# Performance work log

Hardware: AMD Instinct MI355X
Metric: run time of the kernel (lower is better)

Reference implementation:

```python
import jax, jax.numpy as jnp
import numpy as np

HSIZE = 128
E = 640000


def _init_linear(key, fan_in, fan_out):
    # torch nn.Linear default init: U(-1/sqrt(fan_in), 1/sqrt(fan_in))
    kw, kb = jax.random.split(key)
    bound = 1.0 / np.sqrt(fan_in)
    W = jax.random.uniform(kw, (fan_in, fan_out), jnp.float32, -bound, bound)
    b = jax.random.uniform(kb, (fan_out,), jnp.float32, -bound, bound)
    return W, b


def setup_inputs() -> dict:
    key = jax.random.key(0)
    ks = jax.random.split(key, 6)
    hself = jax.random.normal(ks[0], (E, HSIZE), jnp.float32)
    hother = jax.random.normal(ks[1], (E, HSIZE), jnp.float32)
    Wm1, bm1 = _init_linear(ks[2], 2 * HSIZE, HSIZE)
    Wm2, bm2 = _init_linear(ks[3], HSIZE, HSIZE)
    Wu1, bu1 = _init_linear(ks[4], 2 * HSIZE, HSIZE)
    Wu2, bu2 = _init_linear(ks[5], HSIZE, HSIZE)
    return {"hself": hself, "hother": hother,
            "Wm1": Wm1, "bm1": bm1, "Wm2": Wm2, "bm2": bm2,
            "Wu1": Wu1, "bu1": bu1, "Wu2": Wu2, "bu2": bu2}


def _mlp2(a, b, W1, b1, W2, b2):
    # concat([a, b], -1) @ W1 done without materializing the concat
    h = a @ W1[:HSIZE] + b @ W1[HSIZE:] + b1
    h = jax.nn.relu(h)
    return h @ W2 + b2


def reference(hself, hother, Wm1, bm1, Wm2, bm2, Wu1, bu1, Wu2, bu2):
    # msg: Linear(2h,h) -> ReLU -> Linear(h,h) on cat([hself, hother])
    msg = _mlp2(hself, hother, Wm1, bm1, Wm2, bm2)
    # upd: Linear(2h,h) -> ReLU -> Linear(h,h) on cat([hself, msg])
    out = _mlp2(hself, msg, Wu1, bu1, Wu2, bu2)
    return out
```

## Files before the change

### kernel.cpp

```cpp
#include <hip/hip_runtime.h>

typedef __bf16 bf16_t;
typedef __bf16 bf16x8 __attribute__((ext_vector_type(8)));
typedef float f32x4 __attribute__((ext_vector_type(4)));

#define MFMA(a, b, c) __builtin_amdgcn_mfma_f32_16x16x32_bf16((a), (b), (c), 0, 0, 0)

#define E_ROWS 640000
#define BM 128

static __device__ __forceinline__ bf16x8 cvt8(float4 a, float4 b) {
  bf16x8 r;
  r[0] = (bf16_t)a.x; r[1] = (bf16_t)a.y; r[2] = (bf16_t)a.z; r[3] = (bf16_t)a.w;
  r[4] = (bf16_t)b.x; r[5] = (bf16_t)b.y; r[6] = (bf16_t)b.z; r[7] = (bf16_t)b.w;
  return r;
}

static __device__ __forceinline__ unsigned int pk2(float a, float b) {
  unsigned short ua = __builtin_bit_cast(unsigned short, (bf16_t)a);
  unsigned short ub = __builtin_bit_cast(unsigned short, (bf16_t)b);
  return ((unsigned int)ub << 16) | ua;
}

static __device__ __forceinline__ void gload_lds16(const void* g, void* l) {
  __builtin_amdgcn_global_load_lds(
      (const __attribute__((address_space(1))) unsigned int*)g,
      (__attribute__((address_space(3))) unsigned int*)l, 16, 0, 0);
}

__global__ __launch_bounds__(256) void prep_weights(
    const float* __restrict__ Wm1, const float* __restrict__ Wm2,
    const float* __restrict__ Wu1, const float* __restrict__ Wu2,
    bf16_t* __restrict__ wt) {
  int c = blockIdx.x * 256 + threadIdx.x;
  if (c >= 12288) return;
  int lane = c & 63, f = c >> 6;
  const float* W; int base;
  if (f < 64)       { W = Wm1; base = 0;   }
  else if (f < 96)  { W = Wm2; base = 64;  }
  else if (f < 160) { W = Wu1; base = 96;  }
  else              { W = Wu2; base = 160; }
  int fl = f - base;
  int ks = fl >> 3, nb = fl & 7;
  int k0 = 32 * ks + 8 * (lane >> 4);
  int n  = 16 * nb + (lane & 15);
  bf16x8 v;
  #pragma unroll
  for (int j = 0; j < 8; ++j) v[j] = (bf16_t)W[(size_t)(k0 + j) * 128 + n];
  ((bf16x8*)wt)[c] = v;
}

#define STAGE32(dstBase, tc0) { \
  _Pragma("unroll") \
  for (int i_ = 0; i_ < 8; ++i_) \
    gload_lds16((const char*)wt + ((size_t)((tc0) + i_ * 256 + wave * 64 + lane)) * 16, \
                (dstBase) + (i_ * 256 + wave * 64) * 16); }

#define LDW8(s, base, fl0) \
  s##0 = *(const bf16x8*)((base) + ((fl0) + 0) * 1024 + lane * 16); \
  s##1 = *(const bf16x8*)((base) + ((fl0) + 1) * 1024 + lane * 16); \
  s##2 = *(const bf16x8*)((base) + ((fl0) + 2) * 1024 + lane * 16); \
  s##3 = *(const bf16x8*)((base) + ((fl0) + 3) * 1024 + lane * 16); \
  s##4 = *(const bf16x8*)((base) + ((fl0) + 4) * 1024 + lane * 16); \
  s##5 = *(const bf16x8*)((base) + ((fl0) + 5) * 1024 + lane * 16); \
  s##6 = *(const bf16x8*)((base) + ((fl0) + 6) * 1024 + lane * 16); \
  s##7 = *(const bf16x8*)((base) + ((fl0) + 7) * 1024 + lane * 16);

#define ROUND(s, x0, x1) \
  acc00 = MFMA(s##0, x0, acc00); acc10 = MFMA(s##0, x1, acc10); \
  acc01 = MFMA(s##1, x0, acc01); acc11 = MFMA(s##1, x1, acc11); \
  acc02 = MFMA(s##2, x0, acc02); acc12 = MFMA(s##2, x1, acc12); \
  acc03 = MFMA(s##3, x0, acc03); acc13 = MFMA(s##3, x1, acc13); \
  acc04 = MFMA(s##4, x0, acc04); acc14 = MFMA(s##4, x1, acc14); \
  acc05 = MFMA(s##5, x0, acc05); acc15 = MFMA(s##5, x1, acc15); \
  acc06 = MFMA(s##6, x0, acc06); acc16 = MFMA(s##6, x1, acc16); \
  acc07 = MFMA(s##7, x0, acc07); acc17 = MFMA(s##7, x1, acc17);

#define ACCINIT(bp) { const float* bp_ = (bp) + g * 4; float4 q; \
  q = *(const float4*)(bp_ +   0); acc00 = (f32x4){q.x,q.y,q.z,q.w}; acc10 = acc00; \
  q = *(const float4*)(bp_ +  16); acc01 = (f32x4){q.x,q.y,q.z,q.w}; acc11 = acc01; \
  q = *(const float4*)(bp_ +  32); acc02 = (f32x4){q.x,q.y,q.z,q.w}; acc12 = acc02; \
  q = *(const float4*)(bp_ +  48); acc03 = (f32x4){q.x,q.y,q.z,q.w}; acc13 = acc03; \
  q = *(const float4*)(bp_ +  64); acc04 = (f32x4){q.x,q.y,q.z,q.w}; acc14 = acc04; \
  q = *(const float4*)(bp_ +  80); acc05 = (f32x4){q.x,q.y,q.z,q.w}; acc15 = acc05; \
  q = *(const float4*)(bp_ +  96); acc06 = (f32x4){q.x,q.y,q.z,q.w}; acc16 = acc06; \
  q = *(const float4*)(bp_ + 112); acc07 = (f32x4){q.x,q.y,q.z,q.w}; acc17 = acc07; }

#define RPK(av, mt, nb, R) { \
  f32x4 v = av; \
  float e0 = v[0], e1 = v[1], e2 = v[2], e3 = v[3]; \
  if (R) { e0 = fmaxf(e0, 0.f); e1 = fmaxf(e1, 0.f); \
           e2 = fmaxf(e2, 0.f); e3 = fmaxf(e3, 0.f); } \
  uint2 w; w.x = pk2(e0, e1); w.y = pk2(e2, e3); \
  int dl = c + 16 * (2 * ((nb) & 1) + (g >> 1)); \
  *(uint2*)(myrep + (((mt) * 4 + ((nb) >> 1)) * 64 + dl) * 16 + (g & 1) * 8) = w; }

#define RPK_ALL(R) \
  RPK(acc00, 0, 0, R) RPK(acc01, 0, 1, R) RPK(acc02, 0, 2, R) RPK(acc03, 0, 3, R) \
  RPK(acc04, 0, 4, R) RPK(acc05, 0, 5, R) RPK(acc06, 0, 6, R) RPK(acc07, 0, 7, R) \
  RPK(acc10, 1, 0, R) RPK(acc11, 1, 1, R) RPK(acc12, 1, 2, R) RPK(acc13, 1, 3, R) \
  RPK(acc14, 1, 4, R) RPK(acc15, 1, 5, R) RPK(acc16, 1, 6, R) RPK(acc17, 1, 7, R)

#define WAITLDS asm volatile("s_waitcnt lgkmcnt(0)" ::: "memory");
#define VMCNT0  asm volatile("s_waitcnt vmcnt(0)" ::: "memory");

#define RDBX \
  x00 = *(const bf16x8*)(myrep + (0 * 64 + lane) * 16); \
  x01 = *(const bf16x8*)(myrep + (1 * 64 + lane) * 16); \
  x02 = *(const bf16x8*)(myrep + (2 * 64 + lane) * 16); \
  x03 = *(const bf16x8*)(myrep + (3 * 64 + lane) * 16); \
  x10 = *(const bf16x8*)(myrep + (4 * 64 + lane) * 16); \
  x11 = *(const bf16x8*)(myrep + (5 * 64 + lane) * 16); \
  x12 = *(const bf16x8*)(myrep + (6 * 64 + lane) * 16); \
  x13 = *(const bf16x8*)(myrep + (7 * 64 + lane) * 16);

#define LOADX(d0, d1, basep, kk) { \
  float4 a0 = *(const float4*)((basep) + r0 + (kk) * 32); \
  float4 a1 = *(const float4*)((basep) + r0 + (kk) * 32 + 4); \
  float4 b0 = *(const float4*)((basep) + r1 + (kk) * 32); \
  float4 b1 = *(const float4*)((basep) + r1 + (kk) * 32 + 4); \
  d0 = cvt8(a0, a1); d1 = cvt8(b0, b1); }

#define ST(av, mt, nb) { f32x4 v = av; \
  *(float4*)(out + (rowbase + (mt) * 16 + c) * 128 + (nb) * 16 + g * 4) = \
      (float4){v[0], v[1], v[2], v[3]}; }

__global__ __launch_bounds__(256) void fused_mp(
    const float* __restrict__ hself, const float* __restrict__ hother,
    const bf16_t* __restrict__ wt,
    const float* __restrict__ bm1, const float* __restrict__ bm2,
    const float* __restrict__ bu1, const float* __restrict__ bu2,
    float* __restrict__ out) {
  __shared__ char smem[65536];

  const int tid = threadIdx.x;
  const int lane = tid & 63;
  const int wave = tid >> 6;
  const int c = lane & 15;
  const int g = lane >> 4;

  char* WA = smem;
  char* WB = smem + 32768;
  char* myrep = smem + wave * 8192;

  const size_t rowbase = (size_t)blockIdx.x * BM + wave * 32;
  const size_t r0 = (rowbase + c) * 128 + g * 8;
  const size_t r1 = (rowbase + 16 + c) * 128 + g * 8;

  bf16x8 hs00, hs01, hs02, hs03, hs10, hs11, hs12, hs13;
  bf16x8 x00, x01, x02, x03, x10, x11, x12, x13;
  LOADX(hs00, hs10, hself, 0)
  LOADX(hs01, hs11, hself, 1)
  LOADX(hs02, hs12, hself, 2)
  LOADX(hs03, hs13, hself, 3)
  STAGE32(WA, 0)
  STAGE32(WB, 2048)
  LOADX(x00, x10, hother, 0)
  LOADX(x01, x11, hother, 1)
  LOADX(x02, x12, hother, 2)
  LOADX(x03, x13, hother, 3)
  VMCNT0
  __syncthreads();

  f32x4 acc00, acc01, acc02, acc03, acc04, acc05, acc06, acc07;
  f32x4 acc10, acc11, acc12, acc13, acc14, acc15, acc16, acc17;
  bf16x8 wa0, wa1, wa2, wa3, wa4, wa5, wa6, wa7;

  ACCINIT(bm1)
  LDW8(wa, WA, 0)   ROUND(wa, hs00, hs10)
  LDW8(wa, WA, 8)   ROUND(wa, hs01, hs11)
  LDW8(wa, WA, 16)  ROUND(wa, hs02, hs12)
  LDW8(wa, WA, 24)  ROUND(wa, hs03, hs13)
  LDW8(wa, WB, 0)   ROUND(wa, x00, x10)
  LDW8(wa, WB, 8)   ROUND(wa, x01, x11)
  LDW8(wa, WB, 16)  ROUND(wa, x02, x12)
  LDW8(wa, WB, 24)  ROUND(wa, x03, x13)
  __syncthreads();

  STAGE32(WB, 4096)
  RPK_ALL(true)
  WAITLDS
  RDBX
  VMCNT0
  __syncthreads();

  ACCINIT(bm2)
  LDW8(wa, WB, 0)   ROUND(wa, x00, x10)
  LDW8(wa, WB, 8)   ROUND(wa, x01, x11)
  LDW8(wa, WB, 16)  ROUND(wa, x02, x12)
  LDW8(wa, WB, 24)  ROUND(wa, x03, x13)
  __syncthreads();

  STAGE32(WB, 6144)
  RPK_ALL(false)
  WAITLDS
  RDBX
  __syncthreads();

  STAGE32(WA, 8192)
  VMCNT0
  __syncthreads();

  ACCINIT(bu1)
  LDW8(wa, WB, 0)   ROUND(wa, hs00, hs10)
  LDW8(wa, WB, 8)   ROUND(wa, hs01, hs11)
  LDW8(wa, WB, 16)  ROUND(wa, hs02, hs12)
  LDW8(wa, WB, 24)  ROUND(wa, hs03, hs13)
  LDW8(wa, WA, 0)   ROUND(wa, x00, x10)
  LDW8(wa, WA, 8)   ROUND(wa, x01, x11)
  LDW8(wa, WA, 16)  ROUND(wa, x02, x12)
  LDW8(wa, WA, 24)  ROUND(wa, x03, x13)
  __syncthreads();

  STAGE32(WB, 10240)
  RPK_ALL(true)
  WAITLDS
  RDBX
  VMCNT0
  __syncthreads();

  ACCINIT(bu2)
  LDW8(wa, WB, 0)   ROUND(wa, x00, x10)
  LDW8(wa, WB, 8)   ROUND(wa, x01, x11)
  LDW8(wa, WB, 16)  ROUND(wa, x02, x12)
  LDW8(wa, WB, 24)  ROUND(wa, x03, x13)

  ST(acc00, 0, 0) ST(acc01, 0, 1) ST(acc02, 0, 2) ST(acc03, 0, 3)
  ST(acc04, 0, 4) ST(acc05, 0, 5) ST(acc06, 0, 6) ST(acc07, 0, 7)
  ST(acc10, 1, 0) ST(acc11, 1, 1) ST(acc12, 1, 2) ST(acc13, 1, 3)
  ST(acc14, 1, 4) ST(acc15, 1, 5) ST(acc16, 1, 6) ST(acc17, 1, 7)
}

extern "C" void kernel_launch(void* const* d_in, const int* in_sizes, int n_in,
                              void* d_out, int out_size, void* d_ws, size_t ws_size,
                              hipStream_t stream) {
  const float* hself  = (const float*)d_in[0];
  const float* hother = (const float*)d_in[1];
  const float* Wm1 = (const float*)d_in[2];
  const float* bm1 = (const float*)d_in[3];
  const float* Wm2 = (const float*)d_in[4];
  const float* bm2 = (const float*)d_in[5];
  const float* Wu1 = (const float*)d_in[6];
  const float* bu1 = (const float*)d_in[7];
  const float* Wu2 = (const float*)d_in[8];
  const float* bu2 = (const float*)d_in[9];
  float* out = (float*)d_out;
  bf16_t* wt = (bf16_t*)d_ws;

  prep_weights<<<48, 256, 0, stream>>>(Wm1, Wm2, Wu1, Wu2, wt);
  fused_mp<<<E_ROWS / BM, 256, 0, stream>>>(hself, hother, wt,
                                            bm1, bm2, bu1, bu2, out);
}
```

Measured before the change: 360.2 us.

## Double block to 512 threads, stage whole MLP weights at once, per-wave repack

Result: faster. 289.2 us (-19.7%).

```diff
diff --git a/kernel.cpp b/kernel.cpp
--- a/kernel.cpp
+++ b/kernel.cpp
@@ -7,7 +7,7 @@
 #define MFMA(a, b, c) __builtin_amdgcn_mfma_f32_16x16x32_bf16((a), (b), (c), 0, 0, 0)
 
 #define E_ROWS 640000
-#define BM 128
+#define BM 256
 
 static __device__ __forceinline__ bf16x8 cvt8(float4 a, float4 b) {
   bf16x8 r;
@@ -50,11 +50,11 @@
   ((bf16x8*)wt)[c] = v;
 }
 
-#define STAGE32(dstBase, tc0) { \
+#define STAGE96(tc0) { \
   _Pragma("unroll") \
-  for (int i_ = 0; i_ < 8; ++i_) \
-    gload_lds16((const char*)wt + ((size_t)((tc0) + i_ * 256 + wave * 64 + lane)) * 16, \
-                (dstBase) + (i_ * 256 + wave * 64) * 16); }
+  for (int i_ = 0; i_ < 12; ++i_) \
+    gload_lds16((const char*)wt + ((size_t)((tc0) + i_ * 512 + tid)) * 16, \
+                smem + (i_ * 512 + tid) * 16); }
 
 #define LDW8(s, base, fl0) \
   s##0 = *(const bf16x8*)((base) + ((fl0) + 0) * 1024 + lane * 16); \
@@ -86,33 +86,35 @@
   q = *(const float4*)(bp_ +  96); acc06 = (f32x4){q.x,q.y,q.z,q.w}; acc16 = acc06; \
   q = *(const float4*)(bp_ + 112); acc07 = (f32x4){q.x,q.y,q.z,q.w}; acc17 = acc07; }
 
-#define RPK(av, mt, nb, R) { \
+#define RPK_H(av, nb, R) { \
   f32x4 v = av; \
   float e0 = v[0], e1 = v[1], e2 = v[2], e3 = v[3]; \
   if (R) { e0 = fmaxf(e0, 0.f); e1 = fmaxf(e1, 0.f); \
            e2 = fmaxf(e2, 0.f); e3 = fmaxf(e3, 0.f); } \
   uint2 w; w.x = pk2(e0, e1); w.y = pk2(e2, e3); \
   int dl = c + 16 * (2 * ((nb) & 1) + (g >> 1)); \
-  *(uint2*)(myrep + (((mt) * 4 + ((nb) >> 1)) * 64 + dl) * 16 + (g & 1) * 8) = w; }
-
-#define RPK_ALL(R) \
-  RPK(acc00, 0, 0, R) RPK(acc01, 0, 1, R) RPK(acc02, 0, 2, R) RPK(acc03, 0, 3, R) \
-  RPK(acc04, 0, 4, R) RPK(acc05, 0, 5, R) RPK(acc06, 0, 6, R) RPK(acc07, 0, 7, R) \
-  RPK(acc10, 1, 0, R) RPK(acc11, 1, 1, R) RPK(acc12, 1, 2, R) RPK(acc13, 1, 3, R) \
-  RPK(acc14, 1, 4, R) RPK(acc15, 1, 5, R) RPK(acc16, 1, 6, R) RPK(acc17, 1, 7, R)
+  *(uint2*)(myrep + (((nb) >> 1) * 64 + dl) * 16 + (g & 1) * 8) = w; }
 
 #define WAITLDS asm volatile("s_waitcnt lgkmcnt(0)" ::: "memory");
 #define VMCNT0  asm volatile("s_waitcnt vmcnt(0)" ::: "memory");
 
-#define RDBX \
+#define REPACK(R) \
+  RPK_H(acc00, 0, R) RPK_H(acc01, 1, R) RPK_H(acc02, 2, R) RPK_H(acc03, 3, R) \
+  RPK_H(acc04, 4, R) RPK_H(acc05, 5, R) RPK_H(acc06, 6, R) RPK_H(acc07, 7, R) \
+  WAITLDS \
   x00 = *(const bf16x8*)(myrep + (0 * 64 + lane) * 16); \
   x01 = *(const bf16x8*)(myrep + (1 * 64 + lane) * 16); \
   x02 = *(const bf16x8*)(myrep + (2 * 64 + lane) * 16); \
   x03 = *(const bf16x8*)(myrep + (3 * 64 + lane) * 16); \
-  x10 = *(const bf16x8*)(myrep + (4 * 64 + lane) * 16); \
-  x11 = *(const bf16x8*)(myrep + (5 * 64 + lane) * 16); \
-  x12 = *(const bf16x8*)(myrep + (6 * 64 + lane) * 16); \
-  x13 = *(const bf16x8*)(myrep + (7 * 64 + lane) * 16);
+  WAITLDS \
+  RPK_H(acc10, 0, R) RPK_H(acc11, 1, R) RPK_H(acc12, 2, R) RPK_H(acc13, 3, R) \
+  RPK_H(acc14, 4, R) RPK_H(acc15, 5, R) RPK_H(acc16, 6, R) RPK_H(acc17, 7, R) \
+  WAITLDS \
+  x10 = *(const bf16x8*)(myrep + (0 * 64 + lane) * 16); \
+  x11 = *(const bf16x8*)(myrep + (1 * 64 + lane) * 16); \
+  x12 = *(const bf16x8*)(myrep + (2 * 64 + lane) * 16); \
+  x13 = *(const bf16x8*)(myrep + (3 * 64 + lane) * 16); \
+  WAITLDS
 
 #define LOADX(d0, d1, basep, kk) { \
   float4 a0 = *(const float4*)((basep) + r0 + (kk) * 32); \
@@ -125,13 +127,13 @@
   *(float4*)(out + (rowbase + (mt) * 16 + c) * 128 + (nb) * 16 + g * 4) = \
       (float4){v[0], v[1], v[2], v[3]}; }
 
-__global__ __launch_bounds__(256) void fused_mp(
+__global__ __launch_bounds__(512) void fused_mp(
     const float* __restrict__ hself, const float* __restrict__ hother,
     const bf16_t* __restrict__ wt,
     const float* __restrict__ bm1, const float* __restrict__ bm2,
     const float* __restrict__ bu1, const float* __restrict__ bu2,
     float* __restrict__ out) {
-  __shared__ char smem[65536];
+  __shared__ char smem[131072];
 
   const int tid = threadIdx.x;
   const int lane = tid & 63;
@@ -139,9 +141,9 @@
   const int c = lane & 15;
   const int g = lane >> 4;
 
-  char* WA = smem;
-  char* WB = smem + 32768;
-  char* myrep = smem + wave * 8192;
+  char* W1 = smem;
+  char* W2 = smem + 65536;
+  char* myrep = smem + 98304 + wave * 4096;
 
   const size_t rowbase = (size_t)blockIdx.x * BM + wave * 32;
   const size_t r0 = (rowbase + c) * 128 + g * 8;
@@ -153,8 +155,7 @@
   LOADX(hs01, hs11, hself, 1)
   LOADX(hs02, hs12, hself, 2)
   LOADX(hs03, hs13, hself, 3)
-  STAGE32(WA, 0)
-  STAGE32(WB, 2048)
+  STAGE96(0)
   LOADX(x00, x10, hother, 0)
   LOADX(x01, x11, hother, 1)
   LOADX(x02, x12, hother, 2)
@@ -167,63 +168,47 @@
   bf16x8 wa0, wa1, wa2, wa3, wa4, wa5, wa6, wa7;
 
   ACCINIT(bm1)
-  LDW8(wa, WA, 0)   ROUND(wa, hs00, hs10)
-  LDW8(wa, WA, 8)   ROUND(wa, hs01, hs11)
-  LDW8(wa, WA, 16)  ROUND(wa, hs02, hs12)
-  LDW8(wa, WA, 24)  ROUND(wa, hs03, hs13)
-  LDW8(wa, WB, 0)   ROUND(wa, x00, x10)
-  LDW8(wa, WB, 8)   ROUND(wa, x01, x11)
-  LDW8(wa, WB, 16)  ROUND(wa, x02, x12)
-  LDW8(wa, WB, 24)  ROUND(wa, x03, x13)
+  LDW8(wa, W1, 0)   ROUND(wa, hs00, hs10)
+  LDW8(wa, W1, 8)   ROUND(wa, hs01, hs11)
+  LDW8(wa, W1, 16)  ROUND(wa, hs02, hs12)
+  LDW8(wa, W1, 24)  ROUND(wa, hs03, hs13)
+  LDW8(wa, W1, 32)  ROUND(wa, x00, x10)
+  LDW8(wa, W1, 40)  ROUND(wa, x01, x11)
+  LDW8(wa, W1, 48)  ROUND(wa, x02, x12)
+  LDW8(wa, W1, 56)  ROUND(wa, x03, x13)
+
+  REPACK(true)
+
+  ACCINIT(bm2)
+  LDW8(wa, W2, 0)   ROUND(wa, x00, x10)
+  LDW8(wa, W2, 8)   ROUND(wa, x01, x11)
+  LDW8(wa, W2, 16)  ROUND(wa, x02, x12)
+  LDW8(wa, W2, 24)  ROUND(wa, x03, x13)
+
+  REPACK(false)
+
   __syncthreads();
-
-  STAGE32(WB, 4096)
-  RPK_ALL(true)
-  WAITLDS
-  RDBX
+  STAGE96(6144)
   VMCNT0
   __syncthreads();
 
-  ACCINIT(bm2)
-  LDW8(wa, WB, 0)   ROUND(wa, x00, x10)
-  LDW8(wa, WB, 8)   ROUND(wa, x01, x11)
-  LDW8(wa, WB, 16)  ROUND(wa, x02, x12)
-  LDW8(wa, WB, 24)  ROUND(wa, x03, x13)
-  __syncthreads();
-
-  STAGE32(WB, 6144)
-  RPK_ALL(false)
-  WAITLDS
-  RDBX
-  __syncthreads();
-
-  STAGE32(WA, 8192)
-  VMCNT0
-  __syncthreads();
-
   ACCINIT(bu1)
-  LDW8(wa, WB, 0)   ROUND(wa, hs00, hs10)
-  LDW8(wa, WB, 8)   ROUND(wa, hs01, hs11)
-  LDW8(wa, WB, 16)  ROUND(wa, hs02, hs12)
-  LDW8(wa, WB, 24)  ROUND(wa, hs03, hs13)
-  LDW8(wa, WA, 0)   ROUND(wa, x00, x10)
-  LDW8(wa, WA, 8)   ROUND(wa, x01, x11)
-  LDW8(wa, WA, 16)  ROUND(wa, x02, x12)
-  LDW8(wa, WA, 24)  ROUND(wa, x03, x13)
-  __syncthreads();
-
-  STAGE32(WB, 10240)
-  RPK_ALL(true)
-  WAITLDS
-  RDBX
-  VMCNT0
-  __syncthreads();
+  LDW8(wa, W1, 0)   ROUND(wa, hs00, hs10)
+  LDW8(wa, W1, 8)   ROUND(wa, hs01, hs11)
+  LDW8(wa, W1, 16)  ROUND(wa, hs02, hs12)
+  LDW8(wa, W1, 24)  ROUND(wa, hs03, hs13)
+  LDW8(wa, W1, 32)  ROUND(wa, x00, x10)
+  LDW8(wa, W1, 40)  ROUND(wa, x01, x11)
+  LDW8(wa, W1, 48)  ROUND(wa, x02, x12)
+  LDW8(wa, W1, 56)  ROUND(wa, x03, x13)
+
+  REPACK(true)
 
   ACCINIT(bu2)
-  LDW8(wa, WB, 0)   ROUND(wa, x00, x10)
-  LDW8(wa, WB, 8)   ROUND(wa, x01, x11)
-  LDW8(wa, WB, 16)  ROUND(wa, x02, x12)
-  LDW8(wa, WB, 24)  ROUND(wa, x03, x13)
+  LDW8(wa, W2, 0)   ROUND(wa, x00, x10)
+  LDW8(wa, W2, 8)   ROUND(wa, x01, x11)
+  LDW8(wa, W2, 16)  ROUND(wa, x02, x12)
+  LDW8(wa, W2, 24)  ROUND(wa, x03, x13)
 
   ST(acc00, 0, 0) ST(acc01, 0, 1) ST(acc02, 0, 2) ST(acc03, 0, 3)
   ST(acc04, 0, 4) ST(acc05, 0, 5) ST(acc06, 0, 6) ST(acc07, 0, 7)
@@ -248,6 +233,6 @@
   bf16_t* wt = (bf16_t*)d_ws;
 
   prep_weights<<<48, 256, 0, stream>>>(Wm1, Wm2, Wu1, Wu2, wt);
-  fused_mp<<<E_ROWS / BM, 256, 0, stream>>>(hself, hother, wt,
+  fused_mp<<<E_ROWS / BM, 512, 0, stream>>>(hself, hother, wt,
                                             bm1, bm2, bu1, bu2, out);
 }
```
